# Optimization experiments

Measured on AMD Instinct MI355X. Metric: run time of the kernel, lower is better.

The kernel has to match this reference:

```python
import jax, jax.numpy as jnp
import numpy as np

B, N, F, C, K = 8, 256, 64, 16, 2  # batch, agents, hidden_nf, hidden_c (coord channels), category_num
EPS = 1e-4


def _lin(x, W, b=None):
    y = jnp.einsum('...i,oi->...o', x, W)
    return y if b is None else y + b


def _forward(h, coord, vel, category, W_cv, W_e1, b_e1, W_e2, b_e2,
             W_cat1, b_cat1, W_cat2, b_cat2, W_f1, b_f1, W_f2, b_f2,
             W_n1, b_n1, W_n2, b_n2, W_ql, W_kl, W_qm, b_qm):
    relu = jax.nn.relu
    B_, N_, F_ = h.shape
    # --- edge model: dense pairwise features ---
    coord_diff = coord[:, :, None] - coord[:, None]            # [B,N,N,C,3]
    coord_dist = jnp.linalg.norm(coord_diff, axis=-1)          # [B,N,N,C]
    h1 = jnp.broadcast_to(h[:, :, None, :], (B_, N_, N_, F_))
    h2 = jnp.broadcast_to(h[:, None, :, :], (B_, N_, N_, F_))
    edge_h = jnp.concatenate([h1, h2, coord_dist], axis=-1)    # [B,N,N,2F+C]
    edge_feat = relu(_lin(relu(_lin(edge_h, W_e1, b_e1)), W_e2, b_e2))  # [B,N,N,F]
    # --- inner agent attention ---
    att = relu(_lin(h, W_qm, b_qm))[..., None]                 # [B,N,C,1]
    v = coord - jnp.mean(coord, axis=(1, 2), keepdims=True)
    coord = att * v + coord
    # --- reasoning-based coordinate aggregation (loop over K=2 categories) ---
    factors = jnp.zeros(edge_h.shape[:3] + (C,), coord.dtype)
    for i in range(K):
        ci = relu(_lin(relu(_lin(edge_h, W_cat1[i], b_cat1[i])), W_cat2[i], b_cat2[i]))
        factors = factors + category[..., i:i + 1] * ci
    factors = relu(_lin(relu(_lin(factors, W_f1, b_f1)), W_f2, b_f2))   # [B,N,N,C]
    coord = coord + jnp.sum(factors[..., None] * coord_diff, axis=2)    # [B,N,C,3]
    # --- velocity term (linear over channel dim) ---
    coord = coord + jnp.einsum('bncd,oc->bnod', vel, W_cv)
    # --- non-linear equivariant update ---
    cm = jnp.mean(coord, axis=(1, 2), keepdims=True)
    c = coord - cm
    q = jnp.einsum('bncd,oc->bnod', c, W_ql)
    k = jnp.einsum('bncd,oc->bnod', c, W_kl)
    prod = jnp.sum(q * k, axis=-1, keepdims=True)              # [B,N,C,1]
    mask = (prod >= 0).astype(c.dtype)
    kns = jnp.sum(k * k, axis=-1, keepdims=True)
    coord = mask * q + (1 - mask) * (q - prod / (kns + EPS) * k) + cm
    # --- node model: masked sum over neighbors (no self-edge) ---
    nb_mask = 1.0 - jnp.eye(N_, dtype=edge_feat.dtype)
    agg = jnp.einsum('bnmf,nm->bnf', edge_feat, nb_mask)
    h_out = h + _lin(relu(_lin(jnp.concatenate([h, agg], axis=-1), W_n1, b_n1)), W_n2, b_n2)
    return h_out, coord


def setup_inputs() -> dict:
    key = jax.random.key(0)
    ks = jax.random.split(key, 20)
    p = lambda i, shape, fan: jax.random.normal(ks[i], shape, jnp.float32) / np.sqrt(fan)
    z = lambda shape: jnp.zeros(shape, jnp.float32)
    return {
        'h': jax.random.normal(ks[0], (B, N, F), jnp.float32),
        'coord': jax.random.normal(ks[1], (B, N, C, 3), jnp.float32),
        'vel': jax.random.normal(ks[2], (B, N, C, 3), jnp.float32),
        'category': jax.random.uniform(ks[3], (B, N, N, K), jnp.float32),
        'W_cv': p(4, (C, C), C),
        'W_e1': p(5, (F, 2 * F + C), 2 * F + C), 'b_e1': z((F,)),
        'W_e2': p(6, (F, F), F), 'b_e2': z((F,)),
        'W_cat1': p(7, (K, F, 2 * F + C), 2 * F + C), 'b_cat1': z((K, F)),
        'W_cat2': p(8, (K, C, F), F), 'b_cat2': z((K, C)),
        'W_f1': p(9, (C, C), C), 'b_f1': z((C,)),
        'W_f2': p(10, (C, C), C), 'b_f2': z((C,)),
        'W_n1': p(11, (F, 2 * F), 2 * F), 'b_n1': z((F,)),
        'W_n2': p(12, (F, F), F), 'b_n2': z((F,)),
        'W_ql': p(13, (C, C), C),
        'W_kl': p(14, (C, C), C),
        'W_qm': p(15, (C, F), F), 'b_qm': z((C,)),
    }


def reference(h, coord, vel, category, W_cv, W_e1, b_e1, W_e2, b_e2,
              W_cat1, b_cat1, W_cat2, b_cat2, W_f1, b_f1, W_f2, b_f2,
              W_n1, b_n1, W_n2, b_n2, W_ql, W_kl, W_qm, b_qm):
    h_out, coord_out = _forward(h, coord, vel, category, W_cv, W_e1, b_e1, W_e2, b_e2,
                                W_cat1, b_cat1, W_cat2, b_cat2, W_f1, b_f1, W_f2, b_f2,
                                W_n1, b_n1, W_n2, b_n2, W_ql, W_kl, W_qm, b_qm)
    return (h_out, coord_out, category)
```

## Files before the change

kernel.cpp:

```cpp
#include <hip/hip_runtime.h>

typedef unsigned short u16;
typedef unsigned int u32;
typedef _Float16 f16;
typedef __attribute__((ext_vector_type(2))) _Float16 f16x2;
typedef __attribute__((ext_vector_type(4))) _Float16 f16x4;
typedef __attribute__((ext_vector_type(4))) float f32x4;

#define EPSV 1e-4f


static constexpr int WS_FLAG = 0;
static constexpr int WS_ATT  = 16;
static constexpr int WS_CT   = 32784;
static constexpr int WS_AGG  = 131088;
static constexpr int WS_CAC  = 262160;
static constexpr int WS_GWN1 = 360464;
static constexpr int WS_GWN2 = 364560;
static constexpr int WS_BN1  = 372752;
static constexpr int WS_BN2  = 372816;
static constexpr int WS_BIAS = 372880;
static constexpr int WS_GWD  = 373008;
static constexpr int WS_GWE2 = 374544;
static constexpr int WS_GWC2 = 376592;
static constexpr int WS_GWF1 = 377616;
static constexpr int WS_GWF2 = 377744;

static __device__ __forceinline__ float bfld(u16 v) {
  return __uint_as_float(((unsigned)v) << 16);
}
static __device__ __forceinline__ u16 f2b(float x) {
  unsigned u = __float_as_uint(x);
  u += 0x7FFFu + ((u >> 16) & 1u);
  return (u16)(u >> 16);
}
static __device__ __forceinline__ float ldv(const void* p, int i, int flag) {
  return flag ? bfld(((const u16*)p)[i]) : ((const float*)p)[i];
}
static __device__ __forceinline__ void stv(void* p, int i, float v, int flag) {
  if (flag) ((u16*)p)[i] = f2b(v);
  else      ((float*)p)[i] = v;
}
static __device__ __forceinline__ f16* scratchHA(void* outv, int flag) {
  return (f16*)((char*)outv + (size_t)229376 * (flag ? 2 : 4));
}
static __device__ __forceinline__ int sniff_flag(const void* h) {
  const u16* hu = (const u16*)h;
  int cnt = 0;
  for (int i = 0; i < 128; ++i) {
    unsigned e = (hu[i] >> 7) & 0xFFu;
    if ((e >= 100u && e <= 150u) || hu[i] == 0) ++cnt;
  }
  return (cnt >= 112) ? 1 : 0;
}
static __device__ __forceinline__ f16x4 pack4(float a, float b, float c, float d) {
  const f16x2 lo = __builtin_bit_cast(f16x2, __builtin_amdgcn_cvt_pkrtz(a, b));
  const f16x2 hi = __builtin_bit_cast(f16x2, __builtin_amdgcn_cvt_pkrtz(c, d));
  f16x4 r; r[0] = lo[0]; r[1] = lo[1]; r[2] = hi[0]; r[3] = hi[1]; return r;
}
static __device__ __forceinline__ f16x4 pack4_relu(float a, float b, float c, float d) {
  f16x2 lo = __builtin_bit_cast(f16x2, __builtin_amdgcn_cvt_pkrtz(a, b));
  f16x2 hi = __builtin_bit_cast(f16x2, __builtin_amdgcn_cvt_pkrtz(c, d));
  const f16x2 z = {(_Float16)0.f, (_Float16)0.f};
  lo = __builtin_elementwise_max(lo, z);
  hi = __builtin_elementwise_max(hi, z);
  f16x4 r; r[0] = lo[0]; r[1] = lo[1]; r[2] = hi[0]; r[3] = hi[1]; return r;
}
static __device__ __forceinline__ void st8h(f16* dst, uint4 v) {
  uint2 lo; lo.x = v.x; lo.y = v.y;
  uint2 hi; hi.x = v.z; hi.y = v.w;
  *(uint2*)dst = lo;
  *(uint2*)(dst + 4) = hi;
}
static __device__ __forceinline__ void load48(const void* p, int node, int flag,
                                              float* dst) {
  if (flag) {
    const uint4* q4 = (const uint4*)((const u16*)p + node * 48);
#pragma unroll
    for (int c = 0; c < 6; ++c) {
      const uint4 v = q4[c];
      const u32 a[4] = {v.x, v.y, v.z, v.w};
#pragma unroll
      for (int e = 0; e < 4; ++e) {
        dst[c * 8 + e * 2]     = bfld((u16)(a[e] & 0xFFFFu));
        dst[c * 8 + e * 2 + 1] = bfld((u16)(a[e] >> 16));
      }
    }
  } else {
    const float4* q4 = (const float4*)((const float*)p + node * 48);
#pragma unroll
    for (int c = 0; c < 12; ++c) {
      const float4 v = q4[c];
      dst[c * 4] = v.x; dst[c * 4 + 1] = v.y; dst[c * 4 + 2] = v.z; dst[c * 4 + 3] = v.w;
    }
  }
}
static __device__ __forceinline__ void stage_h64(const void* h, int hbase, int flag,
                                                 f16* sH, int tid) {
  if (flag) {
    const uint4* src = (const uint4*)((const u16*)h + hbase);
    for (int v = tid; v < 512; v += 256) {
      const uint4 x = src[v];
      const int e = v * 8;
      f16* dst = &sH[(e >> 6) * 68 + (e & 63)];
      const u32 a[4] = {x.x, x.y, x.z, x.w};
#pragma unroll
      for (int p = 0; p < 4; ++p) {
        dst[p * 2]     = (f16)bfld((u16)(a[p] & 0xFFFFu));
        dst[p * 2 + 1] = (f16)bfld((u16)(a[p] >> 16));
      }
    }
  } else {
    const float4* src = (const float4*)((const float*)h + hbase);
    for (int v = tid; v < 1024; v += 256) {
      const float4 x = src[v];
      const int e = v * 4;
      f16* dst = &sH[(e >> 6) * 68 + (e & 63)];
      dst[0] = (f16)x.x; dst[1] = (f16)x.y; dst[2] = (f16)x.z; dst[3] = (f16)x.w;
    }
  }
}

__global__ __launch_bounds__(256) void k_front(
    const void* __restrict__ h, const void* __restrict__ coord,
    const void* __restrict__ We1, const void* __restrict__ Wc1,
    const void* __restrict__ We2, const void* __restrict__ Wc2,
    const void* __restrict__ Wf1, const void* __restrict__ Wf2,
    const void* __restrict__ Wn1, const void* __restrict__ Wn2,
    const void* __restrict__ Wqm,
    const void* __restrict__ be1, const void* __restrict__ bc1,
    const void* __restrict__ bqm, const void* __restrict__ be2,
    const void* __restrict__ bc2, const void* __restrict__ bf1,
    const void* __restrict__ bf2, const void* __restrict__ bn1,
    const void* __restrict__ bn2,
    float* __restrict__ ws, void* __restrict__ outv) {
  const int blk = blockIdx.x, tid = threadIdx.x;
  __shared__ int sflag;
  if (tid == 0) {
    sflag = sniff_flag(h);
    if (blk == 0) ((int*)ws)[WS_FLAG] = sflag;
  }
  __syncthreads();
  const int flag = sflag;

  if (blk < 8) {
    const int b = blk;
    __shared__ float tile[256 * 49];
    if (flag) {
      const uint4* src = (const uint4*)((const u16*)coord + b * 12288);
      for (int v = tid; v < 1536; v += 256) {
        const uint4 x = src[v];
        const int e = v * 8, node = e / 48, cd = e % 48;
        float* dst = &tile[node * 49 + cd];
        const u32 a[4] = {x.x, x.y, x.z, x.w};
#pragma unroll
        for (int p = 0; p < 4; ++p) {
          dst[p * 2]     = bfld((u16)(a[p] & 0xFFFFu));
          dst[p * 2 + 1] = bfld((u16)(a[p] >> 16));
        }
      }
    } else {
      const float4* src = (const float4*)((const float*)coord + b * 12288);
      for (int v = tid; v < 3072; v += 256) {
        const float4 x = src[v];
        const int e = v * 4, node = e / 48, cd = e % 48;
        float* dst = &tile[node * 49 + cd];
        dst[0] = x.x; dst[1] = x.y; dst[2] = x.z; dst[3] = x.w;
      }
    }
    __syncthreads();
    float* dstb = ws + WS_CT + b * 48 * 256;
    for (int idx = tid; idx < 12288; idx += 256) {
      const int cd = idx >> 8, node = idx & 255;
      dstb[cd * 256 + node] = tile[node * 49 + cd];
    }
    return;
  }
  if (blk < 256) {
    const int t = (blk - 8) * 256 + tid;
    const int STR = 63488;
    f16* gwd  = (f16*)(ws + WS_GWD);
    f16* gwe2 = (f16*)(ws + WS_GWE2);
    f16* gwc2 = (f16*)(ws + WS_GWC2);
    f16* gwf1 = (f16*)(ws + WS_GWF1);
    f16* gwf2 = (f16*)(ws + WS_GWF2);
    for (int idx = t; idx < 3072; idx += STR) {
      const int o = idx >> 4, c = idx & 15;
      const void* src = (o < 64) ? We1 : Wc1;
      const int row = (o < 64) ? o : (o - 64);
      gwd[idx] = (f16)ldv(src, row * 144 + 128 + c, flag);
    }
    for (int idx = t; idx < 4096; idx += STR) gwe2[idx] = (f16)ldv(We2, idx, flag);
    for (int idx = t; idx < 2048; idx += STR) gwc2[idx] = (f16)ldv(Wc2, idx, flag);
    if (t < 256) { gwf1[t] = (f16)ldv(Wf1, t, flag); gwf2[t] = (f16)ldv(Wf2, t, flag); }
    f16* gwn1 = (f16*)(ws + WS_GWN1);
    f16* gwn2 = (f16*)(ws + WS_GWN2);
    for (int idx = t; idx < 8192; idx += STR) gwn1[idx] = (f16)ldv(Wn1, idx, flag);
    for (int idx = t; idx < 4096; idx += STR) gwn2[idx] = (f16)ldv(Wn2, idx, flag);
    if (t < 64)  ws[WS_BN1 + t] = ldv(bn1, t, flag);
    if (t >= 64 && t < 128) ws[WS_BN2 + t - 64] = ldv(bn2, t - 64, flag);
    if (t >= 128 && t < 192) ws[WS_BIAS + t - 128] = ldv(be2, t - 128, flag);
    if (t >= 192 && t < 224) ws[WS_BIAS + 64 + t - 192] = ldv(bc2, t - 192, flag);
    if (t >= 224 && t < 240) ws[WS_BIAS + 96 + t - 224] = ldv(bf1, t - 224, flag);
    if (t >= 240 && t < 256) ws[WS_BIAS + 112 + t - 240] = ldv(bf2, t - 240, flag);
    return;
  }

  const int gb = blk - 256;
  const int nt = gb / 5, grp = gb % 5;
  const int w = tid >> 6, lane = tid & 63;
  const int q = lane >> 4, l15 = lane & 15;
  f16* HA16 = scratchHA(outv, flag);
  f16* HBJ  = HA16 + 2048 * 192;
  __shared__ __align__(16) f16 sW[80 * 68];
  __shared__ __align__(16) f16 sH[64 * 68];
  __shared__ float sBias[80];
  if (flag) {
    for (int idx = tid; idx < 640; idx += 256) {
      const int r = idx >> 3, seg = idx & 7;
      const int row = grp * 80 + r;
      const u16* src;
      if (row < 64)       src = (const u16*)We1 + row * 144;
      else if (row < 192) src = (const u16*)Wc1 + (row - 64) * 144;
      else if (row < 384) {
        const int ro = row - 192;
        src = (ro < 64) ? (const u16*)We1 + ro * 144 + 64
                        : (const u16*)Wc1 + (ro - 64) * 144 + 64;
      } else              src = (const u16*)Wqm + (row - 384) * 64;
      const uint4 v = ((const uint4*)src)[seg];
      const u32 a[4] = {v.x, v.y, v.z, v.w};
      f16* dst = &sW[r * 68 + seg * 8];
#pragma unroll
      for (int p = 0; p < 4; ++p) {
        dst[p * 2]     = (f16)bfld((u16)(a[p] & 0xFFFFu));
        dst[p * 2 + 1] = (f16)bfld((u16)(a[p] >> 16));
      }
    }
  } else {
    for (int idx = tid; idx < 1280; idx += 256) {
      const int r = idx >> 4, seg = idx & 15;
      const int row = grp * 80 + r;
      const float* src;
      if (row < 64)       src = (const float*)We1 + row * 144;
      else if (row < 192) src = (const float*)Wc1 + (row - 64) * 144;
      else if (row < 384) {
        const int ro = row - 192;
        src = (ro < 64) ? (const float*)We1 + ro * 144 + 64
                        : (const float*)Wc1 + (ro - 64) * 144 + 64;
      } else              src = (const float*)Wqm + (row - 384) * 64;
      const float4 v = ((const float4*)src)[seg];
      f16x4 t; t[0] = (f16)v.x; t[1] = (f16)v.y; t[2] = (f16)v.z; t[3] = (f16)v.w;
      *(f16x4*)&sW[r * 68 + seg * 4] = t;
    }
  }
  stage_h64(h, nt * 64 * 64, flag, sH, tid);
  if (tid < 80) {
    const int row = grp * 80 + tid;
    sBias[tid] = (row < 64) ? ldv(be1, row, flag)
               : (row < 192) ? ldv(bc1, row - 64, flag)
               : (row < 384) ? 0.f : ldv(bqm, row - 384, flag);
  }
  __syncthreads();
  f16x4 Af[4];
#pragma unroll
  for (int ks = 0; ks < 4; ++ks)
    Af[ks] = *(const f16x4*)&sH[(w * 16 + l15) * 68 + ks * 16 + q * 4];
#pragma unroll
  for (int ot = 0; ot < 5; ++ot) {
    const float bv = sBias[ot * 16 + l15];
    f32x4 acc = (f32x4){bv, bv, bv, bv};
#pragma unroll
    for (int ks = 0; ks < 4; ++ks) {
      const f16x4 Bf = *(const f16x4*)&sW[(ot * 16 + l15) * 68 + ks * 16 + q * 4];
      acc = __builtin_amdgcn_mfma_f32_16x16x16f16(Af[ks], Bf, acc, 0, 0, 0);
    }
    const int out = grp * 80 + ot * 16 + l15;
    const int nodeD = nt * 64 + w * 16 + q * 4;
#pragma unroll
    for (int r = 0; r < 4; ++r) {
      const int node = nodeD + r;
      if (out < 192) {
        HA16[node * 192 + out] = (f16)acc[r];
      } else if (out < 384) {
        const int ol = out - 192;
        HBJ[(((node >> 8) * 48 + ((ol >> 4) << 2) + ((ol & 15) >> 2)) * 256 +
             (node & 255)) * 4 + (ol & 3)] = (f16)acc[r];
      } else {
        ws[WS_ATT + node * 16 + out - 384] = fmaxf(acc[r], 0.f);
      }
    }
  }
}

__global__ __launch_bounds__(256, 4) void k_edge(const void* __restrict__ cat,
                                                 float* __restrict__ ws,
                                                 void* __restrict__ outv) {
  const int node = ((blockIdx.x & 7) << 8) | (blockIdx.x >> 3);
  const int b = node >> 8, i = node & 255;
  const int tid = threadIdx.x;
  const int w = tid >> 6, lane = tid & 63, q = lane >> 4, l15 = lane & 15;
  const int flag = ((const int*)ws)[WS_FLAG];
  const f16* HA16 = scratchHA(outv, flag);
  const f16* HBJ  = HA16 + 2048 * 192;
  const float* __restrict__ cTb = ws + WS_CT + b * 48 * 256;

  __shared__ __align__(16) f16 sWd[192 * 20];
  __shared__ __align__(16) f16 sWe2[64 * 76];
  __shared__ __align__(16) f16 sWc2[32 * 76];
  __shared__ __align__(16) f16 sWf1[16 * 20];
  __shared__ __align__(16) f16 sWf2[16 * 20];
  __shared__ __align__(16) f16 distS[256 * 20];
  __shared__ float sHa[192];
  __shared__ float sB[128];
  __shared__ __align__(16) float red[448];

  int jj[4]; float mjt[4];
#pragma unroll
  for (int jt = 0; jt < 4; ++jt) {
    jj[jt] = w * 64 + jt * 16 + l15;
    mjt[jt] = (jj[jt] == i) ? 0.f : 1.f;
  }
  const f16* hbq = HBJ + (size_t)(b * 48 + q) * 1024;
  f16x4 hbA[2][4];
#pragma unroll
  for (int og = 0; og < 2; ++og)
#pragma unroll
    for (int jt = 0; jt < 4; ++jt)
      hbA[og][jt] = *(const f16x4*)(hbq + og * 4096 + jj[jt] * 4);

  {
    const u32* gwd = (const u32*)(ws + WS_GWD);
    for (int idx = tid; idx < 1536; idx += 256) {
      const int r = idx >> 3, c = idx & 7;
      *(u32*)&sWd[r * 20 + c * 2] = gwd[idx];
    }
    const u32* gwe = (const u32*)(ws + WS_GWE2);
    for (int idx = tid; idx < 2048; idx += 256) {
      const int r = idx >> 5, c = idx & 31;
      *(u32*)&sWe2[r * 76 + c * 2] = gwe[idx];
    }
    const u32* gwc = (const u32*)(ws + WS_GWC2);
    for (int idx = tid; idx < 1024; idx += 256) {
      const int r = idx >> 5, c = idx & 31;
      *(u32*)&sWc2[r * 76 + c * 2] = gwc[idx];
    }
    if (tid < 128) {
      const int r = tid >> 3, c = tid & 7;
      *(u32*)&sWf1[r * 20 + c * 2] = ((const u32*)(ws + WS_GWF1))[tid];
      *(u32*)&sWf2[r * 20 + c * 2] = ((const u32*)(ws + WS_GWF2))[tid];
    }
    if (tid < 192) sHa[tid] = (float)HA16[node * 192 + tid];
    if (tid < 128) sB[tid] = ws[WS_BIAS + tid];
  }
  {
    float dr[16];
#pragma unroll
    for (int c = 0; c < 16; ++c) {
      float s = 0.f;
#pragma unroll
      for (int d = 0; d < 3; ++d) {
        const int cd = c * 3 + d;
        const float df = cTb[cd * 256 + i] - cTb[cd * 256 + tid];
        s += df * df;
      }
      dr[c] = sqrtf(s);
    }
#pragma unroll
    for (int kk = 0; kk < 4; ++kk)
      *(f16x4*)&distS[tid * 20 + kk * 4] =
          pack4(dr[4 * kk], dr[4 * kk + 1], dr[4 * kk + 2], dr[4 * kk + 3]);
  }
  __syncthreads();

  f16x4 dfr[4];
#pragma unroll
  for (int jt = 0; jt < 4; ++jt)
    dfr[jt] = *(const f16x4*)&distS[jj[jt] * 20 + q * 4];

  f16x4 af[4][4];
#pragma unroll
  for (int og = 0; og < 4; ++og) {
    const f16x4 wd = *(const f16x4*)&sWd[(og * 16 + l15) * 20 + q * 4];
    const float4 sha = *(const float4*)&sHa[og * 16 + q * 4];
#pragma unroll
    for (int jt = 0; jt < 4; ++jt) {
      const f16x4 hb = hbA[og & 1][jt];
      f32x4 a;
      a[0] = sha.x + (float)hb[0];
      a[1] = sha.y + (float)hb[1];
      a[2] = sha.z + (float)hb[2];
      a[3] = sha.w + (float)hb[3];
      a = __builtin_amdgcn_mfma_f32_16x16x16f16(wd, dfr[jt], a, 0, 0, 0);
      af[og][jt] = pack4_relu(a[0], a[1], a[2], a[3]);
      if (og < 2)
        hbA[og & 1][jt] = *(const f16x4*)(hbq + (og + 2) * 4096 + jj[jt] * 4);
    }
  }
  float sagg[4][4];
#pragma unroll
  for (int ft = 0; ft < 4; ++ft) {
    f32x4 C2[4];
#pragma unroll
    for (int jt = 0; jt < 4; ++jt) C2[jt] = (f32x4){0.f, 0.f, 0.f, 0.f};
#pragma unroll
    for (int og = 0; og < 4; ++og) {
      const f16x4 we = *(const f16x4*)&sWe2[(ft * 16 + l15) * 76 + og * 16 + q * 4];
#pragma unroll
      for (int jt = 0; jt < 4; ++jt)
        C2[jt] = __builtin_amdgcn_mfma_f32_16x16x16f16(we, af[og][jt], C2[jt], 0, 0, 0);
    }
#pragma unroll
    for (int r = 0; r < 4; ++r) {
      float s = 0.f;
#pragma unroll
      for (int jt = 0; jt < 4; ++jt)
        s += fmaxf(C2[jt][r] + sB[ft * 16 + q * 4 + r], 0.f) * mjt[jt];
      sagg[ft][r] = s;
    }
  }

  f16x4 hbB[2][4];
#pragma unroll
  for (int g = 0; g < 2; ++g)
#pragma unroll
    for (int jt = 0; jt < 4; ++jt)
      hbB[g][jt] = *(const f16x4*)(hbq + (4 + g) * 4096 + jj[jt] * 4);
  float cv0[4], cv1[4];
#pragma unroll
  for (int jt = 0; jt < 4; ++jt) {
    if (flag) {
      const u32 p = ((const u32*)cat)[node * 256 + jj[jt]];
      cv0[jt] = bfld((u16)(p & 0xFFFFu));
      cv1[jt] = bfld((u16)(p >> 16));
    } else {
      const float2 p = ((const float2*)cat)[node * 256 + jj[jt]];
      cv0[jt] = p.x; cv1[jt] = p.y;
    }
  }

#pragma unroll
  for (int ft = 0; ft < 4; ++ft)
#pragma unroll
    for (int st = 1; st < 16; st <<= 1)
#pragma unroll
      for (int r = 0; r < 4; ++r) sagg[ft][r] += __shfl_xor(sagg[ft][r], st, 64);
  if (l15 == 0) {
#pragma unroll
    for (int ft = 0; ft < 4; ++ft)
#pragma unroll
      for (int r = 0; r < 4; ++r) red[w * 64 + ft * 16 + q * 4 + r] = sagg[ft][r];
  }

  float fac[4][4] = {};
#pragma unroll
  for (int m = 0; m < 2; ++m) {
    f32x4 C3[4];
#pragma unroll
    for (int jt = 0; jt < 4; ++jt) C3[jt] = (f32x4){0.f, 0.f, 0.f, 0.f};
#pragma unroll
    for (int og2 = 0; og2 < 4; ++og2) {
      const int g = m * 4 + og2;
      const int og = 4 + g;
      const f16x4 wd = *(const f16x4*)&sWd[(og * 16 + l15) * 20 + q * 4];
      const f16x4 wc = *(const f16x4*)&sWc2[(m * 16 + l15) * 76 + og2 * 16 + q * 4];
      const float4 sha = *(const float4*)&sHa[og * 16 + q * 4];
#pragma unroll
      for (int jt = 0; jt < 4; ++jt) {
        const f16x4 hb = hbB[g & 1][jt];
        f32x4 a;
        a[0] = sha.x + (float)hb[0];
        a[1] = sha.y + (float)hb[1];
        a[2] = sha.z + (float)hb[2];
        a[3] = sha.w + (float)hb[3];
        a = __builtin_amdgcn_mfma_f32_16x16x16f16(wd, dfr[jt], a, 0, 0, 0);
        const f16x4 afv = pack4_relu(a[0], a[1], a[2], a[3]);
        C3[jt] = __builtin_amdgcn_mfma_f32_16x16x16f16(wc, afv, C3[jt], 0, 0, 0);
        if (g < 6)
          hbB[g & 1][jt] = *(const f16x4*)(hbq + (4 + g + 2) * 4096 + jj[jt] * 4);
      }
    }
#pragma unroll
    for (int jt = 0; jt < 4; ++jt) {
      const float catv = m ? cv1[jt] : cv0[jt];
#pragma unroll
      for (int r = 0; r < 4; ++r)
        fac[jt][r] += catv * fmaxf(C3[jt][r] + sB[64 + m * 16 + q * 4 + r], 0.f);
    }
  }

  const f16x4 w1 = *(const f16x4*)&sWf1[l15 * 20 + q * 4];
  const f16x4 w2 = *(const f16x4*)&sWf2[l15 * 20 + q * 4];
  float civ[12];
#pragma unroll
  for (int r = 0; r < 4; ++r)
#pragma unroll
    for (int d = 0; d < 3; ++d) civ[r * 3 + d] = cTb[(3 * (q * 4 + r) + d) * 256 + i];
  float ca[12] = {};
#pragma unroll
  for (int jt = 0; jt < 4; ++jt) {
    const f16x4 fF = pack4(fac[jt][0], fac[jt][1], fac[jt][2], fac[jt][3]);
    const f32x4 z = {0.f, 0.f, 0.f, 0.f};
    f32x4 G = __builtin_amdgcn_mfma_f32_16x16x16f16(w1, fF, z, 0, 0, 0);
    const f16x4 gF = pack4(fmaxf(G[0] + sB[96 + q * 4 + 0], 0.f),
                           fmaxf(G[1] + sB[96 + q * 4 + 1], 0.f),
                           fmaxf(G[2] + sB[96 + q * 4 + 2], 0.f),
                           fmaxf(G[3] + sB[96 + q * 4 + 3], 0.f));
    f32x4 F2 = __builtin_amdgcn_mfma_f32_16x16x16f16(w2, gF, z, 0, 0, 0);
#pragma unroll
    for (int r = 0; r < 4; ++r) {
      const float fv = fmaxf(F2[r] + sB[112 + q * 4 + r], 0.f);
#pragma unroll
      for (int d = 0; d < 3; ++d) {
        const float cj = cTb[(3 * (q * 4 + r) + d) * 256 + jj[jt]];
        ca[r * 3 + d] += fv * (civ[r * 3 + d] - cj);
      }
    }
  }
#pragma unroll
  for (int st = 1; st < 16; st <<= 1)
#pragma unroll
    for (int u = 0; u < 12; ++u) ca[u] += __shfl_xor(ca[u], st, 64);

  if (l15 == 0) {
#pragma unroll
    for (int u = 0; u < 12; ++u) red[256 + w * 48 + q * 12 + u] = ca[u];
  }
  __syncthreads();
  if (tid < 64) {
    ws[WS_AGG + node * 64 + tid] = red[tid] + red[64 + tid] + red[128 + tid] + red[192 + tid];
  } else if (tid < 112) {
    const int u = tid - 64;
    ws[WS_CAC + node * 48 + u] =
        red[256 + u] + red[256 + 48 + u] + red[256 + 96 + u] + red[256 + 144 + u];
  }
}

__global__ __launch_bounds__(256) void k_epi(const void* __restrict__ h,
                                             const void* __restrict__ coord,
                                             const void* __restrict__ vel,
                                             const void* __restrict__ cat,
                                             const void* __restrict__ Wcv,
                                             const void* __restrict__ Wql,
                                             const void* __restrict__ Wkl,
                                             const float* __restrict__ ws,
                                             void* __restrict__ outv) {
  const int blk = blockIdx.x, tid = threadIdx.x;
  const int flag = ((const int*)ws)[WS_FLAG];
  if (blk < 32) {
    const int w = tid >> 6, lane = tid & 63;
    const int q = lane >> 4, l15 = lane & 15;
    __shared__ __align__(16) f16 sW1[64 * 132];
    __shared__ __align__(16) f16 sW2[64 * 68];
    __shared__ __align__(16) f16 sH[64 * 68];
    __shared__ float sbn[128];
    {
      const uint4* g14 = (const uint4*)(ws + WS_GWN1);
      for (int idx = tid; idx < 1024; idx += 256) {
        const int o = idx >> 4, c8 = idx & 15;
        st8h(&sW1[o * 132 + c8 * 8], g14[idx]);
      }
      const uint4* g24 = (const uint4*)(ws + WS_GWN2);
      for (int idx = tid; idx < 512; idx += 256) {
        const int o = idx >> 3, c8 = idx & 7;
        st8h(&sW2[o * 68 + c8 * 8], g24[idx]);
      }
      stage_h64(h, blk * 64 * 64, flag, sH, tid);
      if (tid < 128) sbn[tid] = (tid < 64) ? ws[WS_BN1 + tid] : ws[WS_BN2 + tid - 64];
    }
    __syncthreads();
    const int node = blk * 64 + w * 16 + l15;
    const int lrow = w * 16 + l15;
    f16x4 xB[8];
#pragma unroll
    for (int kt = 0; kt < 4; ++kt)
      xB[kt] = *(const f16x4*)&sH[lrow * 68 + kt * 16 + q * 4];
#pragma unroll
    for (int kt = 0; kt < 4; ++kt) {
      const float* ap = ws + WS_AGG + node * 64 + kt * 16 + q * 4;
      xB[4 + kt] = pack4(ap[0], ap[1], ap[2], ap[3]);
    }
    f16x4 hidB[4];
#pragma unroll
    for (int ot = 0; ot < 4; ++ot) {
      f32x4 acc;
#pragma unroll
      for (int r = 0; r < 4; ++r) acc[r] = sbn[ot * 16 + q * 4 + r];
#pragma unroll
      for (int kt = 0; kt < 8; ++kt) {
        const f16x4 a = *(const f16x4*)&sW1[(ot * 16 + l15) * 132 + kt * 16 + q * 4];
        acc = __builtin_amdgcn_mfma_f32_16x16x16f16(a, xB[kt], acc, 0, 0, 0);
      }
      hidB[ot] = pack4(fmaxf(acc[0], 0.f), fmaxf(acc[1], 0.f),
                       fmaxf(acc[2], 0.f), fmaxf(acc[3], 0.f));
    }
#pragma unroll
    for (int ft = 0; ft < 4; ++ft) {
      const f16x4 hl = *(const f16x4*)&sH[lrow * 68 + ft * 16 + q * 4];
      f32x4 acc;
#pragma unroll
      for (int r = 0; r < 4; ++r) acc[r] = sbn[64 + ft * 16 + q * 4 + r] + (float)hl[r];
#pragma unroll
      for (int ot = 0; ot < 4; ++ot) {
        const f16x4 a = *(const f16x4*)&sW2[(ft * 16 + l15) * 68 + ot * 16 + q * 4];
        acc = __builtin_amdgcn_mfma_f32_16x16x16f16(a, hidB[ot], acc, 0, 0, 0);
      }
#pragma unroll
      for (int r = 0; r < 4; ++r)
        stv(outv, node * 64 + ft * 16 + q * 4 + r, acc[r], flag);
    }
  } else if (blk < 40) {
    const int b = blk - 32;
    const int n = tid, node = b * 256 + n;
    const int wave = n >> 6, lane = n & 63;
    __shared__ float wcv[256], wql[256], wkl[256];
    __shared__ float redm[16];
    wcv[n] = ldv(Wcv, n, flag);
    wql[n] = ldv(Wql, n, flag);
    wkl[n] = ldv(Wkl, n, flag);
    float cf[48];
    load48(coord, node, flag, cf);
    float s0 = 0.f, s1 = 0.f, s2 = 0.f;
#pragma unroll
    for (int c = 0; c < 16; ++c) { s0 += cf[c*3]; s1 += cf[c*3+1]; s2 += cf[c*3+2]; }
    for (int s = 1; s < 64; s <<= 1) {
      s0 += __shfl_xor(s0, s, 64); s1 += __shfl_xor(s1, s, 64); s2 += __shfl_xor(s2, s, 64);
    }
    if (lane == 0) { redm[wave*4] = s0; redm[wave*4+1] = s1; redm[wave*4+2] = s2; }
    __syncthreads();
    const float m0 = (redm[0]+redm[4]+redm[8]+redm[12]) * (1.f/4096.f);
    const float m1 = (redm[1]+redm[5]+redm[9]+redm[13]) * (1.f/4096.f);
    const float m2 = (redm[2]+redm[6]+redm[10]+redm[14]) * (1.f/4096.f);
    __syncthreads();
    float velf[48];
    load48(vel, node, flag, velf);
    float att[16];
    {
      const float4* ap = (const float4*)(ws + WS_ATT + node * 16);
#pragma unroll
      for (int c4 = 0; c4 < 4; ++c4) {
        const float4 v = ap[c4];
        att[c4*4] = v.x; att[c4*4+1] = v.y; att[c4*4+2] = v.z; att[c4*4+3] = v.w;
      }
    }
    float cac[48];
    {
      const float4* cp = (const float4*)(ws + WS_CAC + node * 48);
#pragma unroll
      for (int c4 = 0; c4 < 12; ++c4) {
        const float4 v = cp[c4];
        cac[c4*4] = v.x; cac[c4*4+1] = v.y; cac[c4*4+2] = v.z; cac[c4*4+3] = v.w;
      }
    }
    float c3[48];
#pragma unroll
    for (int c = 0; c < 16; ++c) {
      const float at = att[c];
#pragma unroll
      for (int d = 0; d < 3; ++d) {
        const int cd = c * 3 + d;
        const float md = (d == 0) ? m0 : ((d == 1) ? m1 : m2);
        float cc = at * (cf[cd] - md) + cf[cd];
        cc += cac[cd];
        float a = cc;
#pragma unroll
        for (int cp = 0; cp < 16; ++cp) a += velf[cp * 3 + d] * wcv[c * 16 + cp];
        c3[cd] = a;
      }
    }
    float t0 = 0.f, t1 = 0.f, t2 = 0.f;
#pragma unroll
    for (int c = 0; c < 16; ++c) { t0 += c3[c*3]; t1 += c3[c*3+1]; t2 += c3[c*3+2]; }
    for (int s = 1; s < 64; s <<= 1) {
      t0 += __shfl_xor(t0, s, 64); t1 += __shfl_xor(t1, s, 64); t2 += __shfl_xor(t2, s, 64);
    }
    if (lane == 0) { redm[wave*4] = t0; redm[wave*4+1] = t1; redm[wave*4+2] = t2; }
    __syncthreads();
    const float cm0 = (redm[0]+redm[4]+redm[8]+redm[12]) * (1.f/4096.f);
    const float cm1 = (redm[1]+redm[5]+redm[9]+redm[13]) * (1.f/4096.f);
    const float cm2 = (redm[2]+redm[6]+redm[10]+redm[14]) * (1.f/4096.f);
    float cc[48];
#pragma unroll
    for (int c = 0; c < 16; ++c) {
      cc[c*3]   = c3[c*3]   - cm0;
      cc[c*3+1] = c3[c*3+1] - cm1;
      cc[c*3+2] = c3[c*3+2] - cm2;
    }
#pragma unroll
    for (int o = 0; o < 16; ++o) {
      float qv[3], kv[3];
#pragma unroll
      for (int d = 0; d < 3; ++d) {
        float sq = 0.f, sk = 0.f;
#pragma unroll
        for (int cp = 0; cp < 16; ++cp) {
          sq += cc[cp * 3 + d] * wql[o * 16 + cp];
          sk += cc[cp * 3 + d] * wkl[o * 16 + cp];
        }
        qv[d] = sq; kv[d] = sk;
      }
      const float prod = qv[0]*kv[0] + qv[1]*kv[1] + qv[2]*kv[2];
      const float kns  = kv[0]*kv[0] + kv[1]*kv[1] + kv[2]*kv[2];
      const float wq = prod / (kns + EPSV);
#pragma unroll
      for (int d = 0; d < 3; ++d) {
        const float cmd = (d == 0) ? cm0 : ((d == 1) ? cm1 : cm2);
        const float val = (prod >= 0.f) ? qv[d] : (qv[d] - wq * kv[d]);
        stv(outv, 131072 + node * 48 + o * 3 + d, val + cmd, flag);
      }
    }
  } else {
    const int idx = (blk - 40) * 256 + tid;
    if (flag) {
      ((uint4*)((char*)outv + 458752))[idx] = ((const uint4*)cat)[idx];
    } else {
      ((uint4*)((char*)outv + 917504))[idx] = ((const uint4*)cat)[idx];
      ((uint4*)((char*)outv + 917504))[idx + 131072] = ((const uint4*)cat)[idx + 131072];
    }
  }
}

extern "C" void kernel_launch(void* const* d_in, const int* in_sizes, int n_in,
                              void* d_out, int out_size, void* d_ws, size_t ws_size,
                              hipStream_t stream) {
  (void)in_sizes; (void)n_in; (void)out_size; (void)ws_size;
  const void* h    = d_in[0];
  const void* coord= d_in[1];
  const void* vel  = d_in[2];
  const void* cat  = d_in[3];
  const void* Wcv  = d_in[4];
  const void* We1  = d_in[5];
  const void* be1  = d_in[6];
  const void* We2  = d_in[7];
  const void* be2  = d_in[8];
  const void* Wc1  = d_in[9];
  const void* bc1  = d_in[10];
  const void* Wc2  = d_in[11];
  const void* bc2  = d_in[12];
  const void* Wf1  = d_in[13];
  const void* bf1v = d_in[14];
  const void* Wf2  = d_in[15];
  const void* bf2v = d_in[16];
  const void* Wn1  = d_in[17];
  const void* bn1  = d_in[18];
  const void* Wn2  = d_in[19];
  const void* bn2  = d_in[20];
  const void* Wql  = d_in[21];
  const void* Wkl  = d_in[22];
  const void* Wqm  = d_in[23];
  const void* bqm  = d_in[24];
  float* ws = (float*)d_ws;

  k_front<<<416, 256, 0, stream>>>(h, coord, We1, Wc1, We2, Wc2, Wf1, Wf2,
                                   Wn1, Wn2, Wqm, be1, bc1, bqm, be2, bc2,
                                   bf1v, bf2v, bn1, bn2, ws, d_out);
  k_edge<<<2048, 256, 0, stream>>>(cat, ws, d_out);
  k_epi<<<552, 256, 0, stream>>>(h, coord, vel, cat, Wcv, Wql, Wkl, ws, d_out);
}
```

Measured before the change: 174.6 us.

## Process two nodes per k_edge block and shrink coord-transpose tile

Each k_edge block now handles two source nodes (i and i+128) in a loop, so the shared-memory weight staging is amortized over two nodes and the grid is halved. The k_front coord transpose now runs in four 64-node chunks with a smaller shared tile, which reduces that kernel's LDS footprint. In exchange each block runs longer and does an extra sync and distance recompute per block, and there are fewer blocks available to hide latency.

```diff
diff --git a/kernel.cpp b/kernel.cpp
--- a/kernel.cpp
+++ b/kernel.cpp
@@ -145,34 +145,37 @@
 
   if (blk < 8) {
     const int b = blk;
-    __shared__ float tile[256 * 49];
-    if (flag) {
-      const uint4* src = (const uint4*)((const u16*)coord + b * 12288);
-      for (int v = tid; v < 1536; v += 256) {
-        const uint4 x = src[v];
-        const int e = v * 8, node = e / 48, cd = e % 48;
-        float* dst = &tile[node * 49 + cd];
-        const u32 a[4] = {x.x, x.y, x.z, x.w};
-#pragma unroll
-        for (int p = 0; p < 4; ++p) {
-          dst[p * 2]     = bfld((u16)(a[p] & 0xFFFFu));
-          dst[p * 2 + 1] = bfld((u16)(a[p] >> 16));
+    __shared__ float tile[64 * 49];
+    float* dstb = ws + WS_CT + b * 48 * 256;
+    for (int g = 0; g < 4; ++g) {
+      if (g) __syncthreads();
+      if (flag) {
+        const uint4* src = (const uint4*)((const u16*)coord + b * 12288 + g * 3072);
+        for (int v = tid; v < 384; v += 256) {
+          const uint4 x = src[v];
+          const int e = v * 8, nl = e / 48, cd = e % 48;
+          float* dst = &tile[nl * 49 + cd];
+          const u32 a[4] = {x.x, x.y, x.z, x.w};
+#pragma unroll
+          for (int p = 0; p < 4; ++p) {
+            dst[p * 2]     = bfld((u16)(a[p] & 0xFFFFu));
+            dst[p * 2 + 1] = bfld((u16)(a[p] >> 16));
+          }
         }
-      }
-    } else {
-      const float4* src = (const float4*)((const float*)coord + b * 12288);
-      for (int v = tid; v < 3072; v += 256) {
-        const float4 x = src[v];
-        const int e = v * 4, node = e / 48, cd = e % 48;
-        float* dst = &tile[node * 49 + cd];
-        dst[0] = x.x; dst[1] = x.y; dst[2] = x.z; dst[3] = x.w;
-      }
-    }
-    __syncthreads();
-    float* dstb = ws + WS_CT + b * 48 * 256;
-    for (int idx = tid; idx < 12288; idx += 256) {
-      const int cd = idx >> 8, node = idx & 255;
-      dstb[cd * 256 + node] = tile[node * 49 + cd];
+      } else {
+        const float4* src = (const float4*)((const float*)coord + b * 12288 + g * 3072);
+        for (int v = tid; v < 768; v += 256) {
+          const float4 x = src[v];
+          const int e = v * 4, nl = e / 48, cd = e % 48;
+          float* dst = &tile[nl * 49 + cd];
+          dst[0] = x.x; dst[1] = x.y; dst[2] = x.z; dst[3] = x.w;
+        }
+      }
+      __syncthreads();
+      for (int idx = tid; idx < 3072; idx += 256) {
+        const int cd = idx >> 6, nl = idx & 63;
+        dstb[cd * 256 + g * 64 + nl] = tile[nl * 49 + cd];
+      }
     }
     return;
   }
@@ -295,8 +298,8 @@
 __global__ __launch_bounds__(256, 4) void k_edge(const void* __restrict__ cat,
                                                  float* __restrict__ ws,
                                                  void* __restrict__ outv) {
-  const int node = ((blockIdx.x & 7) << 8) | (blockIdx.x >> 3);
-  const int b = node >> 8, i = node & 255;
+  const int b = blockIdx.x & 7;
+  const int ih = blockIdx.x >> 3;
   const int tid = threadIdx.x;
   const int w = tid >> 6, lane = tid & 63, q = lane >> 4, l15 = lane & 15;
   const int flag = ((const int*)ws)[WS_FLAG];
@@ -310,16 +313,13 @@
   __shared__ __align__(16) f16 sWf1[16 * 20];
   __shared__ __align__(16) f16 sWf2[16 * 20];
   __shared__ __align__(16) f16 distS[256 * 20];
-  __shared__ float sHa[192];
+  __shared__ __align__(16) float sHaB[384];
   __shared__ float sB[128];
   __shared__ __align__(16) float red[448];
 
-  int jj[4]; float mjt[4];
-#pragma unroll
-  for (int jt = 0; jt < 4; ++jt) {
-    jj[jt] = w * 64 + jt * 16 + l15;
-    mjt[jt] = (jj[jt] == i) ? 0.f : 1.f;
-  }
+  int jj[4];
+#pragma unroll
+  for (int jt = 0; jt < 4; ++jt) jj[jt] = w * 64 + jt * 16 + l15;
   const f16* hbq = HBJ + (size_t)(b * 48 + q) * 1024;
   f16x4 hbA[2][4];
 #pragma unroll
@@ -349,7 +349,11 @@
       *(u32*)&sWf1[r * 20 + c * 2] = ((const u32*)(ws + WS_GWF1))[tid];
       *(u32*)&sWf2[r * 20 + c * 2] = ((const u32*)(ws + WS_GWF2))[tid];
     }
-    if (tid < 192) sHa[tid] = (float)HA16[node * 192 + tid];
+    if (tid < 192) {
+      const int n0 = (b << 8) | ih;
+      sHaB[tid]       = (float)HA16[n0 * 192 + tid];
+      sHaB[192 + tid] = (float)HA16[(n0 + 128) * 192 + tid];
+    }
     if (tid < 128) sB[tid] = ws[WS_BIAS + tid];
   }
   {
@@ -360,7 +364,7 @@
 #pragma unroll
       for (int d = 0; d < 3; ++d) {
         const int cd = c * 3 + d;
-        const float df = cTb[cd * 256 + i] - cTb[cd * 256 + tid];
+        const float df = cTb[cd * 256 + ih] - cTb[cd * 256 + tid];
         s += df * df;
       }
       dr[c] = sqrtf(s);
@@ -372,166 +376,202 @@
   }
   __syncthreads();
 
-  f16x4 dfr[4];
-#pragma unroll
-  for (int jt = 0; jt < 4; ++jt)
-    dfr[jt] = *(const f16x4*)&distS[jj[jt] * 20 + q * 4];
-
-  f16x4 af[4][4];
-#pragma unroll
-  for (int og = 0; og < 4; ++og) {
-    const f16x4 wd = *(const f16x4*)&sWd[(og * 16 + l15) * 20 + q * 4];
-    const float4 sha = *(const float4*)&sHa[og * 16 + q * 4];
-#pragma unroll
-    for (int jt = 0; jt < 4; ++jt) {
-      const f16x4 hb = hbA[og & 1][jt];
-      f32x4 a;
-      a[0] = sha.x + (float)hb[0];
-      a[1] = sha.y + (float)hb[1];
-      a[2] = sha.z + (float)hb[2];
-      a[3] = sha.w + (float)hb[3];
-      a = __builtin_amdgcn_mfma_f32_16x16x16f16(wd, dfr[jt], a, 0, 0, 0);
-      af[og][jt] = pack4_relu(a[0], a[1], a[2], a[3]);
-      if (og < 2)
-        hbA[og & 1][jt] = *(const f16x4*)(hbq + (og + 2) * 4096 + jj[jt] * 4);
-    }
-  }
-  float sagg[4][4];
-#pragma unroll
-  for (int ft = 0; ft < 4; ++ft) {
-    f32x4 C2[4];
-#pragma unroll
-    for (int jt = 0; jt < 4; ++jt) C2[jt] = (f32x4){0.f, 0.f, 0.f, 0.f};
+#pragma unroll 1
+  for (int half = 0; half < 2; ++half) {
+    const int i = ih | (half << 7);
+    const int node = (b << 8) | i;
+    if (half) {
+      __syncthreads();
+#pragma unroll
+      for (int og = 0; og < 2; ++og)
+#pragma unroll
+        for (int jt = 0; jt < 4; ++jt)
+          hbA[og][jt] = *(const f16x4*)(hbq + og * 4096 + jj[jt] * 4);
+      float dr[16];
+#pragma unroll
+      for (int c = 0; c < 16; ++c) {
+        float s = 0.f;
+#pragma unroll
+        for (int d = 0; d < 3; ++d) {
+          const int cd = c * 3 + d;
+          const float df = cTb[cd * 256 + i] - cTb[cd * 256 + tid];
+          s += df * df;
+        }
+        dr[c] = sqrtf(s);
+      }
+#pragma unroll
+      for (int kk = 0; kk < 4; ++kk)
+        *(f16x4*)&distS[tid * 20 + kk * 4] =
+            pack4(dr[4 * kk], dr[4 * kk + 1], dr[4 * kk + 2], dr[4 * kk + 3]);
+      __syncthreads();
+    }
+    float mjt[4];
+#pragma unroll
+    for (int jt = 0; jt < 4; ++jt) mjt[jt] = (jj[jt] == i) ? 0.f : 1.f;
+    const float* sHa = sHaB + half * 192;
+
+    f16x4 dfr[4];
+#pragma unroll
+    for (int jt = 0; jt < 4; ++jt)
+      dfr[jt] = *(const f16x4*)&distS[jj[jt] * 20 + q * 4];
+
+    f16x4 af[4][4];
 #pragma unroll
     for (int og = 0; og < 4; ++og) {
-      const f16x4 we = *(const f16x4*)&sWe2[(ft * 16 + l15) * 76 + og * 16 + q * 4];
-#pragma unroll
-      for (int jt = 0; jt < 4; ++jt)
-        C2[jt] = __builtin_amdgcn_mfma_f32_16x16x16f16(we, af[og][jt], C2[jt], 0, 0, 0);
-    }
-#pragma unroll
-    for (int r = 0; r < 4; ++r) {
-      float s = 0.f;
-#pragma unroll
-      for (int jt = 0; jt < 4; ++jt)
-        s += fmaxf(C2[jt][r] + sB[ft * 16 + q * 4 + r], 0.f) * mjt[jt];
-      sagg[ft][r] = s;
-    }
-  }
-
-  f16x4 hbB[2][4];
-#pragma unroll
-  for (int g = 0; g < 2; ++g)
-#pragma unroll
-    for (int jt = 0; jt < 4; ++jt)
-      hbB[g][jt] = *(const f16x4*)(hbq + (4 + g) * 4096 + jj[jt] * 4);
-  float cv0[4], cv1[4];
-#pragma unroll
-  for (int jt = 0; jt < 4; ++jt) {
-    if (flag) {
-      const u32 p = ((const u32*)cat)[node * 256 + jj[jt]];
-      cv0[jt] = bfld((u16)(p & 0xFFFFu));
-      cv1[jt] = bfld((u16)(p >> 16));
-    } else {
-      const float2 p = ((const float2*)cat)[node * 256 + jj[jt]];
-      cv0[jt] = p.x; cv1[jt] = p.y;
-    }
-  }
-
-#pragma unroll
-  for (int ft = 0; ft < 4; ++ft)
-#pragma unroll
-    for (int st = 1; st < 16; st <<= 1)
-#pragma unroll
-      for (int r = 0; r < 4; ++r) sagg[ft][r] += __shfl_xor(sagg[ft][r], st, 64);
-  if (l15 == 0) {
-#pragma unroll
-    for (int ft = 0; ft < 4; ++ft)
-#pragma unroll
-      for (int r = 0; r < 4; ++r) red[w * 64 + ft * 16 + q * 4 + r] = sagg[ft][r];
-  }
-
-  float fac[4][4] = {};
-#pragma unroll
-  for (int m = 0; m < 2; ++m) {
-    f32x4 C3[4];
-#pragma unroll
-    for (int jt = 0; jt < 4; ++jt) C3[jt] = (f32x4){0.f, 0.f, 0.f, 0.f};
-#pragma unroll
-    for (int og2 = 0; og2 < 4; ++og2) {
-      const int g = m * 4 + og2;
-      const int og = 4 + g;
       const f16x4 wd = *(const f16x4*)&sWd[(og * 16 + l15) * 20 + q * 4];
-      const f16x4 wc = *(const f16x4*)&sWc2[(m * 16 + l15) * 76 + og2 * 16 + q * 4];
       const float4 sha = *(const float4*)&sHa[og * 16 + q * 4];
 #pragma unroll
       for (int jt = 0; jt < 4; ++jt) {
-        const f16x4 hb = hbB[g & 1][jt];
+        const f16x4 hb = hbA[og & 1][jt];
         f32x4 a;
         a[0] = sha.x + (float)hb[0];
         a[1] = sha.y + (float)hb[1];
         a[2] = sha.z + (float)hb[2];
         a[3] = sha.w + (float)hb[3];
         a = __builtin_amdgcn_mfma_f32_16x16x16f16(wd, dfr[jt], a, 0, 0, 0);
-        const f16x4 afv = pack4_relu(a[0], a[1], a[2], a[3]);
-        C3[jt] = __builtin_amdgcn_mfma_f32_16x16x16f16(wc, afv, C3[jt], 0, 0, 0);
-        if (g < 6)
-          hbB[g & 1][jt] = *(const f16x4*)(hbq + (4 + g + 2) * 4096 + jj[jt] * 4);
-      }
-    }
+        af[og][jt] = pack4_relu(a[0], a[1], a[2], a[3]);
+        if (og < 2)
+          hbA[og & 1][jt] = *(const f16x4*)(hbq + (og + 2) * 4096 + jj[jt] * 4);
+      }
+    }
+    float sagg[4][4];
+#pragma unroll
+    for (int ft = 0; ft < 4; ++ft) {
+      f32x4 C2[4];
+#pragma unroll
+      for (int jt = 0; jt < 4; ++jt) C2[jt] = (f32x4){0.f, 0.f, 0.f, 0.f};
+#pragma unroll
+      for (int og = 0; og < 4; ++og) {
+        const f16x4 we = *(const f16x4*)&sWe2[(ft * 16 + l15) * 76 + og * 16 + q * 4];
+#pragma unroll
+        for (int jt = 0; jt < 4; ++jt)
+          C2[jt] = __builtin_amdgcn_mfma_f32_16x16x16f16(we, af[og][jt], C2[jt], 0, 0, 0);
+      }
+#pragma unroll
+      for (int r = 0; r < 4; ++r) {
+        float s = 0.f;
+#pragma unroll
+        for (int jt = 0; jt < 4; ++jt)
+          s += fmaxf(C2[jt][r] + sB[ft * 16 + q * 4 + r], 0.f) * mjt[jt];
+        sagg[ft][r] = s;
+      }
+    }
+
+    f16x4 hbB[2][4];
+#pragma unroll
+    for (int g = 0; g < 2; ++g)
+#pragma unroll
+      for (int jt = 0; jt < 4; ++jt)
+        hbB[g][jt] = *(const f16x4*)(hbq + (4 + g) * 4096 + jj[jt] * 4);
+    float cv0[4], cv1[4];
 #pragma unroll
     for (int jt = 0; jt < 4; ++jt) {
-      const float catv = m ? cv1[jt] : cv0[jt];
-#pragma unroll
-      for (int r = 0; r < 4; ++r)
-        fac[jt][r] += catv * fmaxf(C3[jt][r] + sB[64 + m * 16 + q * 4 + r], 0.f);
-    }
-  }
-
-  const f16x4 w1 = *(const f16x4*)&sWf1[l15 * 20 + q * 4];
-  const f16x4 w2 = *(const f16x4*)&sWf2[l15 * 20 + q * 4];
-  float civ[12];
-#pragma unroll
-  for (int r = 0; r < 4; ++r)
-#pragma unroll
-    for (int d = 0; d < 3; ++d) civ[r * 3 + d] = cTb[(3 * (q * 4 + r) + d) * 256 + i];
-  float ca[12] = {};
-#pragma unroll
-  for (int jt = 0; jt < 4; ++jt) {
-    const f16x4 fF = pack4(fac[jt][0], fac[jt][1], fac[jt][2], fac[jt][3]);
-    const f32x4 z = {0.f, 0.f, 0.f, 0.f};
-    f32x4 G = __builtin_amdgcn_mfma_f32_16x16x16f16(w1, fF, z, 0, 0, 0);
-    const f16x4 gF = pack4(fmaxf(G[0] + sB[96 + q * 4 + 0], 0.f),
-                           fmaxf(G[1] + sB[96 + q * 4 + 1], 0.f),
-                           fmaxf(G[2] + sB[96 + q * 4 + 2], 0.f),
-                           fmaxf(G[3] + sB[96 + q * 4 + 3], 0.f));
-    f32x4 F2 = __builtin_amdgcn_mfma_f32_16x16x16f16(w2, gF, z, 0, 0, 0);
-#pragma unroll
-    for (int r = 0; r < 4; ++r) {
-      const float fv = fmaxf(F2[r] + sB[112 + q * 4 + r], 0.f);
-#pragma unroll
-      for (int d = 0; d < 3; ++d) {
-        const float cj = cTb[(3 * (q * 4 + r) + d) * 256 + jj[jt]];
-        ca[r * 3 + d] += fv * (civ[r * 3 + d] - cj);
-      }
-    }
-  }
-#pragma unroll
-  for (int st = 1; st < 16; st <<= 1)
-#pragma unroll
-    for (int u = 0; u < 12; ++u) ca[u] += __shfl_xor(ca[u], st, 64);
-
-  if (l15 == 0) {
-#pragma unroll
-    for (int u = 0; u < 12; ++u) red[256 + w * 48 + q * 12 + u] = ca[u];
-  }
-  __syncthreads();
-  if (tid < 64) {
-    ws[WS_AGG + node * 64 + tid] = red[tid] + red[64 + tid] + red[128 + tid] + red[192 + tid];
-  } else if (tid < 112) {
-    const int u = tid - 64;
-    ws[WS_CAC + node * 48 + u] =
-        red[256 + u] + red[256 + 48 + u] + red[256 + 96 + u] + red[256 + 144 + u];
+      if (flag) {
+        const u32 p = ((const u32*)cat)[node * 256 + jj[jt]];
+        cv0[jt] = bfld((u16)(p & 0xFFFFu));
+        cv1[jt] = bfld((u16)(p >> 16));
+      } else {
+        const float2 p = ((const float2*)cat)[node * 256 + jj[jt]];
+        cv0[jt] = p.x; cv1[jt] = p.y;
+      }
+    }
+
+#pragma unroll
+    for (int ft = 0; ft < 4; ++ft)
+#pragma unroll
+      for (int st = 1; st < 16; st <<= 1)
+#pragma unroll
+        for (int r = 0; r < 4; ++r) sagg[ft][r] += __shfl_xor(sagg[ft][r], st, 64);
+    if (l15 == 0) {
+#pragma unroll
+      for (int ft = 0; ft < 4; ++ft)
+#pragma unroll
+        for (int r = 0; r < 4; ++r) red[w * 64 + ft * 16 + q * 4 + r] = sagg[ft][r];
+    }
+
+    float fac[4][4] = {};
+#pragma unroll
+    for (int m = 0; m < 2; ++m) {
+      f32x4 C3[4];
+#pragma unroll
+      for (int jt = 0; jt < 4; ++jt) C3[jt] = (f32x4){0.f, 0.f, 0.f, 0.f};
+#pragma unroll
+      for (int og2 = 0; og2 < 4; ++og2) {
+        const int g = m * 4 + og2;
+        const int og = 4 + g;
+        const f16x4 wd = *(const f16x4*)&sWd[(og * 16 + l15) * 20 + q * 4];
+        const f16x4 wc = *(const f16x4*)&sWc2[(m * 16 + l15) * 76 + og2 * 16 + q * 4];
+        const float4 sha = *(const float4*)&sHa[og * 16 + q * 4];
+#pragma unroll
+        for (int jt = 0; jt < 4; ++jt) {
+          const f16x4 hb = hbB[g & 1][jt];
+          f32x4 a;
+          a[0] = sha.x + (float)hb[0];
+          a[1] = sha.y + (float)hb[1];
+          a[2] = sha.z + (float)hb[2];
+          a[3] = sha.w + (float)hb[3];
+          a = __builtin_amdgcn_mfma_f32_16x16x16f16(wd, dfr[jt], a, 0, 0, 0);
+          const f16x4 afv = pack4_relu(a[0], a[1], a[2], a[3]);
+          C3[jt] = __builtin_amdgcn_mfma_f32_16x16x16f16(wc, afv, C3[jt], 0, 0, 0);
+          if (g < 6)
+            hbB[g & 1][jt] = *(const f16x4*)(hbq + (4 + g + 2) * 4096 + jj[jt] * 4);
+        }
+      }
+#pragma unroll
+      for (int jt = 0; jt < 4; ++jt) {
+        const float catv = m ? cv1[jt] : cv0[jt];
+#pragma unroll
+        for (int r = 0; r < 4; ++r)
+          fac[jt][r] += catv * fmaxf(C3[jt][r] + sB[64 + m * 16 + q * 4 + r], 0.f);
+      }
+    }
+
+    const f16x4 w1 = *(const f16x4*)&sWf1[l15 * 20 + q * 4];
+    const f16x4 w2 = *(const f16x4*)&sWf2[l15 * 20 + q * 4];
+    float civ[12];
+#pragma unroll
+    for (int r = 0; r < 4; ++r)
+#pragma unroll
+      for (int d = 0; d < 3; ++d) civ[r * 3 + d] = cTb[(3 * (q * 4 + r) + d) * 256 + i];
+    float ca[12] = {};
+#pragma unroll
+    for (int jt = 0; jt < 4; ++jt) {
+      const f16x4 fF = pack4(fac[jt][0], fac[jt][1], fac[jt][2], fac[jt][3]);
+      const f32x4 z = {0.f, 0.f, 0.f, 0.f};
+      f32x4 G = __builtin_amdgcn_mfma_f32_16x16x16f16(w1, fF, z, 0, 0, 0);
+      const f16x4 gF = pack4(fmaxf(G[0] + sB[96 + q * 4 + 0], 0.f),
+                             fmaxf(G[1] + sB[96 + q * 4 + 1], 0.f),
+                             fmaxf(G[2] + sB[96 + q * 4 + 2], 0.f),
+                             fmaxf(G[3] + sB[96 + q * 4 + 3], 0.f));
+      f32x4 F2 = __builtin_amdgcn_mfma_f32_16x16x16f16(w2, gF, z, 0, 0, 0);
+#pragma unroll
+      for (int r = 0; r < 4; ++r) {
+        const float fv = fmaxf(F2[r] + sB[112 + q * 4 + r], 0.f);
+#pragma unroll
+        for (int d = 0; d < 3; ++d) {
+          const float cj = cTb[(3 * (q * 4 + r) + d) * 256 + jj[jt]];
+          ca[r * 3 + d] += fv * (civ[r * 3 + d] - cj);
+        }
+      }
+    }
+#pragma unroll
+    for (int st = 1; st < 16; st <<= 1)
+#pragma unroll
+      for (int u = 0; u < 12; ++u) ca[u] += __shfl_xor(ca[u], st, 64);
+
+    if (l15 == 0) {
+#pragma unroll
+      for (int u = 0; u < 12; ++u) red[256 + w * 48 + q * 12 + u] = ca[u];
+    }
+    __syncthreads();
+    if (tid < 64) {
+      ws[WS_AGG + node * 64 + tid] =
+          red[tid] + red[64 + tid] + red[128 + tid] + red[192 + tid];
+    } else if (tid < 112) {
+      const int u = tid - 64;
+      ws[WS_CAC + node * 48 + u] =
+          red[256 + u] + red[256 + 48 + u] + red[256 + 96 + u] + red[256 + 144 + u];
+    }
   }
 }
 
@@ -753,6 +793,6 @@
   k_front<<<416, 256, 0, stream>>>(h, coord, We1, Wc1, We2, Wc2, Wf1, Wf2,
                                    Wn1, Wn2, Wqm, be1, bc1, bqm, be2, bc2,
                                    bf1v, bf2v, bn1, bn2, ws, d_out);
-  k_edge<<<2048, 256, 0, stream>>>(cat, ws, d_out);
+  k_edge<<<1024, 256, 0, stream>>>(cat, ws, d_out);
   k_epi<<<552, 256, 0, stream>>>(h, coord, vel, cat, Wcv, Wql, Wkl, ws, d_out);
 }
```

Result: slower. 424.2 us (+142.9%).
